# Performance work log

Hardware: AMD Instinct MI355X
Metric: run time of the kernel (lower is better)

Reference implementation:

```python
import jax, jax.numpy as jnp
import numpy as np

B, SEQ, S, DIM_IN, DIM_K, DIM_V = 4, 2048, 128, 512, 64, 64
L = SEQ + 2 * S
NEG = -1e30  # stand-in for log(0) in the tril mask (finite for stable vjp)


def _layernorm(x, g, b, eps=1e-5):
    m = jnp.mean(x, axis=-1, keepdims=True)
    v = jnp.var(x, axis=-1, keepdims=True)
    return (x - m) / jnp.sqrt(v + eps) * g + b


def setup_inputs() -> dict:
    key = jax.random.key(0)
    ks = jax.random.split(key, 18)
    w = lambda k, shape, s=0.02: (jax.random.normal(k, shape, jnp.float32) * s)
    inp = {
        "x": jax.random.normal(ks[0], (B, L, DIM_IN), jnp.float32),
        "Wq": w(ks[1], (DIM_IN, DIM_K)),
        "Wk": w(ks[2], (DIM_IN, DIM_K)),
        "Wv": w(ks[3], (DIM_IN, DIM_V)),
        "Wq_s": w(ks[4], (DIM_IN, DIM_K)),
        "Wk_s": w(ks[5], (DIM_IN, DIM_K)),
        "Wv_s": w(ks[6], (DIM_IN, DIM_V)),
        "Wq_e": w(ks[7], (DIM_IN, DIM_K)),
        "Wk_e": w(ks[8], (DIM_IN, DIM_K)),
        "Wv_e": w(ks[9], (DIM_IN, DIM_V)),
        "ln_g": jnp.ones((DIM_IN,), jnp.float32),
        "ln_b": jnp.zeros((DIM_IN,), jnp.float32),
        "ln_s_g": jnp.ones((DIM_IN,), jnp.float32),
        "ln_s_b": jnp.zeros((DIM_IN,), jnp.float32),
        "ln_e_g": jnp.ones((DIM_IN,), jnp.float32),
        "ln_e_b": jnp.zeros((DIM_IN,), jnp.float32),
        "cope_emb": jax.random.normal(ks[10], (DIM_K, S), jnp.float32),
        "offset": 0,
    }
    return inp


def reference(x, Wq, Wk, Wv, Wq_s, Wk_s, Wv_s, Wq_e, Wk_e, Wv_e,
              ln_g, ln_b, ln_s_g, ln_s_b, ln_e_g, ln_e_b, cope_emb, offset):
    # extract_state: first/last state_len tokens
    xs, xm, xe = x[:, :S], x[:, S:L - S], x[:, -S:]
    xm = _layernorm(xm, ln_g, ln_b)
    xs = _layernorm(xs, ln_s_g, ln_s_b)
    xe = _layernorm(xe, ln_e_g, ln_e_b)

    q, k, v = xm @ Wq, xm @ Wk, xm @ Wv          # (B, SEQ, dk/dv)
    q_s, k_s, v_s = xs @ Wq_s, xs @ Wk_s, xs @ Wv_s
    q_e, k_e, v_e = xe @ Wq_e, xe @ Wk_e, xe @ Wv_e

    # CoPE bias over the non-state block
    logits = jnp.einsum('bqd,bkd->bqk', q, k)    # (B, SEQ, SEQ)
    gates = jax.nn.sigmoid(logits)
    pos = jnp.flip(jnp.cumsum(jnp.flip(gates, -1), axis=-1), -1)
    pos = jnp.minimum(pos, jnp.float32(S - 1))
    pos_ceil = jnp.ceil(pos).astype(jnp.int32)
    pos_floor = jnp.floor(pos).astype(jnp.int32)
    logits_int = jnp.einsum('bqd,dk->bqk', q, cope_emb)  # (B, SEQ, S)
    logits_c = jnp.take_along_axis(logits_int, pos_ceil, axis=-1)
    logits_f = jnp.take_along_axis(logits_int, pos_floor, axis=-1)
    wfrac = pos - pos_floor.astype(pos.dtype)
    bias = logits_c * wfrac + logits_f * (1.0 - wfrac)   # (B, SEQ, SEQ)

    q_full = jnp.concatenate([q_s, q, q_e], axis=1)      # (B, L, dk)
    k_full = jnp.concatenate([k_s, k, k_e], axis=1)
    v_full = jnp.concatenate([v_s, v, v_e], axis=1)

    # explicit tril log-mask bias with CoPE injected in the middle block
    tri = jnp.tril(jnp.ones((L, L), dtype=bool))
    attn_bias = jnp.where(tri, 0.0, NEG).astype(jnp.float32)
    attn_bias = jnp.broadcast_to(attn_bias, (B, L, L))
    attn_bias = attn_bias.at[:, S:L - S, S:L - S].add(bias)

    scale = 1.0 / jnp.sqrt(jnp.float32(DIM_K))
    scores = jnp.einsum('bqd,bkd->bqk', q_full, k_full) * scale + attn_bias
    att = jax.nn.softmax(scores, axis=-1)
    return jnp.einsum('bqk,bkd->bqd', att, v_full)       # (B, L, dv)
```

## Files before the change

kernel.cpp:

```cpp
#include <hip/hip_runtime.h>
#include <math.h>

#define B_    4
#define SEQ_  2048
#define S_    128
#define L_    2304
#define DIN   512
#define DK    64
#define NEGINF (-1e30f)
#define SCALE 0.125f
#define NCOLS 2176
#define NMID  8192
#define NEDGE 1024
#define LE    2304
#define PROWS 4352

typedef _Float16 f16;
typedef __attribute__((ext_vector_type(8))) _Float16 half8;
typedef __attribute__((ext_vector_type(4))) float f32x4;

union U4 { uint4 u; f16 h[8]; };

__global__ __launch_bounds__(256) void k_ln(
    const float* __restrict__ x,
    const float* __restrict__ g0, const float* __restrict__ b0,
    const float* __restrict__ gs, const float* __restrict__ bs,
    const float* __restrict__ ge, const float* __restrict__ be,
    f16* __restrict__ xh, f16* __restrict__ xl)
{
    const int wave = threadIdx.x >> 6, lane = threadIdx.x & 63;
    const int row  = blockIdx.x * 4 + wave;
    const float4* xr = (const float4*)(x + (size_t)row * DIN);
    float4 v0 = xr[lane], v1 = xr[lane + 64];
    float s  = v0.x + v0.y + v0.z + v0.w + v1.x + v1.y + v1.z + v1.w;
    float s2 = v0.x*v0.x + v0.y*v0.y + v0.z*v0.z + v0.w*v0.w
             + v1.x*v1.x + v1.y*v1.y + v1.z*v1.z + v1.w*v1.w;
    #pragma unroll
    for (int m = 1; m < 64; m <<= 1) { s += __shfl_xor(s, m); s2 += __shfl_xor(s2, m); }
    float mean = s * (1.f / DIN);
    float var  = s2 * (1.f / DIN) - mean * mean;
    float rstd = rsqrtf(var + 1e-5f);

    const int r = row % L_;
    const float *gg, *bb;
    if (r < S_)            { gg = gs; bb = bs; }
    else if (r >= L_ - S_) { gg = ge; bb = be; }
    else                   { gg = g0; bb = b0; }
    float4 ga = ((const float4*)gg)[lane], gb = ((const float4*)gg)[lane + 64];
    float4 ba = ((const float4*)bb)[lane], bb4 = ((const float4*)bb)[lane + 64];

    float n0[4], n1[4];
    n0[0] = (v0.x - mean) * rstd * ga.x + ba.x;
    n0[1] = (v0.y - mean) * rstd * ga.y + ba.y;
    n0[2] = (v0.z - mean) * rstd * ga.z + ba.z;
    n0[3] = (v0.w - mean) * rstd * ga.w + ba.w;
    n1[0] = (v1.x - mean) * rstd * gb.x + bb4.x;
    n1[1] = (v1.y - mean) * rstd * gb.y + bb4.y;
    n1[2] = (v1.z - mean) * rstd * gb.z + bb4.z;
    n1[3] = (v1.w - mean) * rstd * gb.w + bb4.w;

    union { uint2 u; f16 h[4]; } h0, h1, l0, l1;
    #pragma unroll
    for (int i = 0; i < 4; ++i) {
        h0.h[i] = (f16)n0[i]; l0.h[i] = (f16)(n0[i] - (float)h0.h[i]);
        h1.h[i] = (f16)n1[i]; l1.h[i] = (f16)(n1[i] - (float)h1.h[i]);
    }
    f16* ph = xh + (size_t)row * DIN;
    f16* pl = xl + (size_t)row * DIN;
    *(uint2*)(ph + 4 * lane)       = h0.u;
    *(uint2*)(ph + 256 + 4 * lane) = h1.u;
    *(uint2*)(pl + 4 * lane)       = l0.u;
    *(uint2*)(pl + 256 + 4 * lane) = l1.u;
}

// ... 57 lines not shown
        __syncthreads();
        #pragma unroll
        for (int h = 0; h < 2; ++h) {
            half8 ah[2], al[2], bh[2], bl[2];
            #pragma unroll
            for (int rs = 0; rs < 2; ++rs) {
                const f16* base = As + (r0 + 16 * rs + cl) * 136 + h * 32 + quad * 8;
                ah[rs] = *(const half8*)(base);
                al[rs] = *(const half8*)(base + 64);
            }
            #pragma unroll
            for (int cs = 0; cs < 2; ++cs) {
                const f16* base = Bs + (c0 + 16 * cs + cl) * 136 + h * 32 + quad * 8;
                bh[cs] = *(const half8*)(base);
                bl[cs] = *(const half8*)(base + 64);
            }
            #pragma unroll
            for (int rs = 0; rs < 2; ++rs)
                #pragma unroll
                for (int cs = 0; cs < 2; ++cs) {
                    acc[rs][cs] = __builtin_amdgcn_mfma_f32_16x16x32_f16(ah[rs], bh[cs], acc[rs][cs], 0, 0, 0);
                    if (m < 2) {
                        acc[rs][cs] = __builtin_amdgcn_mfma_f32_16x16x32_f16(ah[rs], bl[cs], acc[rs][cs], 0, 0, 0);
                        acc[rs][cs] = __builtin_amdgcn_mfma_f32_16x16x32_f16(al[rs], bh[cs], acc[rs][cs], 0, 0, 0);
                    }
                }
        }
    }

    const int bI = row0 / L_;
    const int rb = row0 - bI * L_;
    f16* sp = (m == 0) ? qsp : ksp;
    #pragma unroll
    for (int rs = 0; rs < 2; ++rs)
        #pragma unroll
        for (int cs = 0; cs < 2; ++cs)
            #pragma unroll
            for (int r = 0; r < 4; ++r) {
                int lrow = r0 + 16 * rs + quad * 4 + r;
                int col  = c0 + 16 * cs + cl;
                float v  = acc[rs][cs][r];
                size_t grow = (size_t)(row0 + lrow);
                outf[grow * DK + col] = v;
                if (m < 2) {
                    f16 hv = (f16)v;
                    sp[grow * 128 + col]      = hv;
                    sp[grow * 128 + 64 + col] = (f16)(v - (float)hv);
                } else {
                    vhT[(size_t)(bI * 64 + col) * L_ + rb + lrow] = (f16)v;
                }
            }
}

__global__ __launch_bounds__(256) void k_dots(
    const f16* __restrict__ qsp, const f16* __restrict__ ksp,
    float* __restrict__ D)
{
    __shared__ f16 Qs[128 * 136];
    __shared__ f16 Ks[64 * 136];
    const int tid  = threadIdx.x;
    const int gr0  = blockIdx.x * 128;
    const int col0 = blockIdx.y * 64;
    const int b    = gr0 >> 11;
    const size_t qrow0 = (size_t)b * L_ + S_ + (gr0 & 2047);
    const size_t krow0 = (size_t)b * L_ + col0;

    #pragma unroll
    for (int i = 0; i < 8; ++i) {
        int g = tid + 256 * i;
        int r = g >> 4, c = g & 15;
        *(uint4*)(Qs + r * 136 + c * 8) = *(const uint4*)(qsp + (qrow0 + r) * 128 + c * 8);
    }
    #pragma unroll
    for (int i = 0; i < 4; ++i) {
        int g = tid + 256 * i;
        int r = g >> 4, c = g & 15;
        *(uint4*)(Ks + r * 136 + c * 8) = *(const uint4*)(ksp + (krow0 + r) * 128 + c * 8);
    }
    __syncthreads();

    const int w = tid >> 6, lane = tid & 63;
    const int cl = lane & 15, quad = lane >> 4;

    f32x4 acc[2][4];
    #pragma unroll
    for (int i = 0; i < 2; ++i)
        #pragma unroll
        for (int j = 0; j < 4; ++j) acc[i][j] = 0.f;

    #pragma unroll
    for (int h = 0; h < 2; ++h) {
        half8 ah[2], al[2], bh[4], bl[4];
        #pragma unroll
        for (int rs = 0; rs < 2; ++rs) {
            const f16* base = Qs + (32 * w + 16 * rs + cl) * 136 + h * 32 + quad * 8;
            ah[rs] = *(const half8*)(base);
            al[rs] = *(const half8*)(base + 64);
        }
        #pragma unroll
        for (int c = 0; c < 4; ++c) {
            const f16* base = Ks + (16 * c + cl) * 136 + h * 32 + quad * 8;
            bh[c] = *(const half8*)(base);
            bl[c] = *(const half8*)(base + 64);
        }
        #pragma unroll
        for (int rs = 0; rs < 2; ++rs)
            #pragma unroll
            for (int c = 0; c < 4; ++c) {
                acc[rs][c] = __builtin_amdgcn_mfma_f32_16x16x32_f16(ah[rs], bh[c], acc[rs][c], 0, 0, 0);
                acc[rs][c] = __builtin_amdgcn_mfma_f32_16x16x32_f16(ah[rs], bl[c], acc[rs][c], 0, 0, 0);
                acc[rs][c] = __builtin_amdgcn_mfma_f32_16x16x32_f16(al[rs], bh[c], acc[rs][c], 0, 0, 0);
            }
    }

    #pragma unroll
    for (int rs = 0; rs < 2; ++rs)
        #pragma unroll
        for (int c = 0; c < 4; ++c)
            #pragma unroll
            for (int r = 0; r < 4; ++r) {
                int mrow = gr0 + 32 * w + 16 * rs + quad * 4 + r;
                int n    = col0 + 16 * c + cl;
                D[(size_t)mrow * NCOLS + n] = acc[rs][c][r];
            }
}

__global__ __launch_bounds__(256) void k_scan(
    const float* __restrict__ qf, const float* __restrict__ cope,
    float* __restrict__ D)
{
    __shared__ float qv[DK];
    __shared__ float li[128];
    __shared__ float red[256];
    __shared__ float wtot[4];
    const int tid = threadIdx.x;
    const int gr  = blockIdx.x;
    const int b   = gr >> 11;
    const int q   = gr & 2047;
    const size_t grow = (size_t)b * L_ + S_ + q;

    if (tid < 16) ((float4*)qv)[tid] = ((const float4*)qf)[grow * 16 + tid];
    __syncthreads();
    if (tid < 128) {
        float a = 0.f;
        #pragma unroll
        for (int d = 0; d < DK; ++d) a += qv[d] * cope[d * S_ + tid];
        li[tid] = a;
    }

    const float* Dr = D + (size_t)gr * NCOLS;
    const int j0 = tid * 8;
    float dot[8], gte[8];
    *(float4*)&dot[0] = *(const float4*)(Dr + 128 + j0);
    *(float4*)&dot[4] = *(const float4*)(Dr + 128 + j0 + 4);
    float sv = (tid < 128) ? Dr[tid] * SCALE : NEGINF;

    float csum = 0.f;
    #pragma unroll
    for (int jj = 0; jj < 8; ++jj) {
        gte[jj] = 1.f / (1.f + __expf(-dot[jj]));
        csum += gte[jj];
    }
    const int lane = tid & 63, wid = tid >> 6;
    float inc = csum;
    #pragma unroll
    for (int off = 1; off < 64; off <<= 1) {
        float u = __shfl_down(inc, off, 64);
        if (lane + off < 64) inc += u;
    }
    if (lane == 0) wtot[wid] = inc;
    __syncthreads();
    float wsuf = 0.f;
    #pragma unroll
    for (int w = 0; w < 4; ++w) if (w > wid) wsuf += wtot[w];
    float run = inc - csum + wsuf;

    float p8[8];
    #pragma unroll
    for (int jj = 7; jj >= 0; --jj) {
        run += gte[jj];
        float pos = fminf(run, (float)(S_ - 1));
        float pfl = floorf(pos);
        int ic  = (int)ceilf(pos);
        int ifl = (int)pfl;
        float w = pos - pfl;
        float bias = li[ic] * w + li[ifl] * (1.f - w);
        p8[jj] = (j0 + jj <= q) ? dot[jj] * SCALE + bias : NEGINF;
    }

    float mx = sv;
    #pragma unroll
    for (int jj = 0; jj < 8; ++jj) mx = fmaxf(mx, p8[jj]);
    red[tid] = mx;
    __syncthreads();
    for (int off = 128; off > 0; off >>= 1) {
        if (tid < off) red[tid] = fmaxf(red[tid], red[tid + off]);
        __syncthreads();
    }
    mx = red[0];
    __syncthreads();

    float lsum = 0.f;
    float e8[8];
    #pragma unroll
    for (int jj = 0; jj < 8; ++jj) {
        e8[jj] = __expf(p8[jj] - mx);
        lsum += e8[jj];
    }
    float es = 0.f;
    if (tid < 128) { es = __expf(sv - mx); lsum += es; }
    red[tid] = lsum;
    __syncthreads();
    for (int off = 128; off > 0; off >>= 1) {
        if (tid < off) red[tid] += red[tid + off];
        __syncthreads();
    }
    float inv = 1.f / red[0];

    f16* pb = (f16*)D + (size_t)gr * PROWS;
    const int qlim = (q & ~63) + 64;
    if (j0 < qlim) {
        U4 o;
        #pragma unroll
        for (int jj = 0; jj < 8; ++jj) o.h[jj] = (f16)(e8[jj] * inv);
        *(uint4*)(pb + 128 + j0) = o.u;
    }
    if (tid < 128) pb[tid] = (f16)(es * inv);
}

__global__ __launch_bounds__(256) void k_pv(
    const f16* __restrict__ Pb, const f16* __restrict__ vhT,
    float* __restrict__ Opart)
{
    __shared__ f16 Ps[64 * 72];
    __shared__ f16 Vt[64 * 72];
    const int tid = threadIdx.x;
    const int gr0 = blockIdx.x * 64;
    const int ks  = blockIdx.y;
    const int b   = gr0 >> 11, q0 = gr0 & 2047;
    const int cmax  = (191 + q0) >> 6;
    const int c_beg = ks * 9;
    int c_end = c_beg + 9;
    if (c_end > 34) c_end = 34;
    if (c_end > cmax + 1) c_end = cmax + 1;

    const int w = tid >> 6, lane = tid & 63;
    const int cl = lane & 15, quad = lane >> 4;
    f32x4 acc[4];
    #pragma unroll
    for (int c = 0; c < 4; ++c) acc[c] = 0.f;

    for (int ch = c_beg; ch < c_end; ++ch) {
        __syncthreads();
        #pragma unroll
        for (int i = 0; i < 2; ++i) {
            int g = tid + 256 * i;
            int r = g >> 3, c = g & 7;
            *(uint4*)(Ps + r * 72 + c * 8) =
                *(const uint4*)(Pb + (size_t)(gr0 + r) * PROWS + ch * 64 + c * 8);
            *(uint4*)(Vt + r * 72 + c * 8) =
                *(const uint4*)(vhT + (size_t)(b * 64 + r) * L_ + ch * 64 + c * 8);
        }
        __syncthreads();
        #pragma unroll
        for (int h = 0; h < 2; ++h) {
            half8 a = *(const half8*)(Ps + (16 * w + cl) * 72 + h * 32 + quad * 8);
            #pragma unroll
            for (int c = 0; c < 4; ++c) {
                half8 bv = *(const half8*)(Vt + (16 * c + cl) * 72 + h * 32 + quad * 8);
                acc[c] = __builtin_amdgcn_mfma_f32_16x16x32_f16(a, bv, acc[c], 0, 0, 0);
            }
        }
    }
    #pragma unroll
    for (int c = 0; c < 4; ++c)
        #pragma unroll
        for (int r = 0; r < 4; ++r) {
            int mrow = gr0 + 16 * w + quad * 4 + r;
            int n    = 16 * c + cl;
            Opart[((size_t)ks * NMID + mrow) * DK + n] = acc[c][r];
        }
}

__global__ __launch_bounds__(256) void k_merge(
    const float* __restrict__ Opart, float* __restrict__ out)
{
    const int e  = blockIdx.x * 256 + threadIdx.x;
    const int gr = e >> 6, c = e & 63;
    const int b  = gr >> 11, q = gr & 2047;
    const int NP = NMID * DK;
    float s = Opart[e] + Opart[e + NP] + Opart[e + 2 * NP] + Opart[e + 3 * NP];
    out[((size_t)b * L_ + S_ + q) * DK + c] = s;
}

__global__ __launch_bounds__(256) void k_dots_edge(
    const float* __restrict__ qf, const float* __restrict__ kf,
    float* __restrict__ De)
{
    const int bx   = blockIdx.x;
    const int b    = bx >> 1;
    const int half = bx & 1;
    const int col0 = blockIdx.y * 128;
    if (half == 0 && col0 > 127) return;

    __shared__ float Qs[128 * 68];
    __shared__ float Kt[64 * 136];
    const int tid = threadIdx.x;
    const int er0 = bx * 128;
    const size_t qrow0 = (size_t)b * L_ + (half ? 2176 : 0);
    const size_t krow0 = (size_t)b * L_ + col0;

    #pragma unroll
    for (int i = 0; i < 8; ++i) {
        int g = tid + 256 * i;
        int r = g >> 4, f = g & 15;
        *(float4*)(Qs + r * 68 + f * 4) = ((const float4*)qf)[(qrow0 + r) * 16 + f];
    }
    #pragma unroll
    for (int i = 0; i < 8; ++i) {
        int g = tid + 256 * i;
        int j = g >> 4, f = g & 15;
        float4 kv = ((const float4*)kf)[(krow0 + j) * 16 + f];
        Kt[(f * 4 + 0) * 136 + j] = kv.x;
        Kt[(f * 4 + 1) * 136 + j] = kv.y;
        Kt[(f * 4 + 2) * 136 + j] = kv.z;
        Kt[(f * 4 + 3) * 136 + j] = kv.w;
    }
    __syncthreads();

    const int c8 = tid & 15, r8 = tid >> 4;
    float acc[8][8] = {};
    for (int d0 = 0; d0 < 64; d0 += 4) {
        float4 a[8];
        #pragma unroll
        for (int i = 0; i < 8; ++i)
            a[i] = *(const float4*)(Qs + (r8 * 8 + i) * 68 + d0);
        #pragma unroll
        for (int dd = 0; dd < 4; ++dd) {
            float4 k0 = *(const float4*)(Kt + (d0 + dd) * 136 + c8 * 8);
            float4 k1 = *(const float4*)(Kt + (d0 + dd) * 136 + c8 * 8 + 4);
            #pragma unroll
            for (int i = 0; i < 8; ++i) {
                float av = (dd == 0) ? a[i].x : (dd == 1) ? a[i].y : (dd == 2) ? a[i].z : a[i].w;
                acc[i][0] += av * k0.x; acc[i][1] += av * k0.y;
                acc[i][2] += av * k0.z; acc[i][3] += av * k0.w;
                acc[i][4] += av * k1.x; acc[i][5] += av * k1.y;
                acc[i][6] += av * k1.z; acc[i][7] += av * k1.w;
            }
        }
    }
    #pragma unroll
    for (int i = 0; i < 8; ++i) {
        size_t o = (size_t)(er0 + r8 * 8 + i) * LE + col0 + c8 * 8;
        *(float4*)(De + o)     = make_float4(acc[i][0], acc[i][1], acc[i][2], acc[i][3]);
        *(float4*)(De + o + 4) = make_float4(acc[i][4], acc[i][5], acc[i][6], acc[i][7]);
    }
}

__global__ __launch_bounds__(256) void k_soft_edge(float* __restrict__ De)
{
    __shared__ float red[256];
    const int tid = threadIdx.x;
    const int er  = blockIdx.x;
    const int r   = er & 255;
    const int Q   = (r < 128) ? r : (2048 + r);
    const size_t rowoff = (size_t)er * LE;

    float v[9];
    #pragma unroll
    for (int i = 0; i < 9; ++i) {
        int j = tid + 256 * i;
        float d = De[rowoff + j];
        v[i] = (j <= Q) ? d * SCALE : NEGINF;
    }
    float mx = v[0];
    #pragma unroll
    for (int i = 1; i < 9; ++i) mx = fmaxf(mx, v[i]);
    red[tid] = mx;
    __syncthreads();
    for (int off = 128; off > 0; off >>= 1) {
        if (tid < off) red[tid] = fmaxf(red[tid], red[tid + off]);
        __syncthreads();
    }
    mx = red[0];
    __syncthreads();

    float lsum = 0.f;
    #pragma unroll
    for (int i = 0; i < 9; ++i) {
        v[i] = __expf(v[i] - mx);
        lsum += v[i];
    }
    red[tid] = lsum;
    __syncthreads();
    for (int off = 128; off > 0; off >>= 1) {
        if (tid < off) red[tid] += red[tid + off];
        __syncthreads();
    }
    float inv = 1.f / red[0];
    #pragma unroll
    for (int i = 0; i < 9; ++i)
        De[rowoff + tid + 256 * i] = v[i] * inv;
}

__global__ __launch_bounds__(256) void k_pv_edge(
    const float* __restrict__ De, const float* __restrict__ vf,
    float* __restrict__ Oe)
{
    __shared__ float Ps[32 * 68];
    __shared__ float Vs[64 * 68];
    const int tid = threadIdx.x;
    const int er0 = blockIdx.x * 32;
    const int ks  = blockIdx.y;
    const int b   = er0 >> 8, r0 = er0 & 255;
    const int Qmax = (r0 < 128) ? (r0 + 31) : (2048 + r0 + 31);
    const int cmax = Qmax >> 6;
    const int c_beg = ks * 9;
    int c_end = c_beg + 9;
    if (c_end > 36) c_end = 36;
    if (c_end > cmax + 1) c_end = cmax + 1;

    const int c4 = tid & 15, rg = tid >> 4;
    float acc[2][4] = {};

    for (int ch = c_beg; ch < c_end; ++ch) {
        __syncthreads();
        #pragma unroll
        for (int i = 0; i < 2; ++i) {
            int g = tid + 256 * i;
            int r = g >> 4, f = g & 15;
            *(float4*)(Ps + r * 68 + f * 4) =
                *(const float4*)(De + (size_t)(er0 + r) * LE + ch * 64 + f * 4);
        }
        #pragma unroll
        for (int i = 0; i < 4; ++i) {
            int g = tid + 256 * i;
            int j = g >> 4, f = g & 15;
            *(float4*)(Vs + j * 68 + f * 4) =
                *(const float4*)(vf + (size_t)(b * L_ + ch * 64 + j) * DK + f * 4);
        }
        __syncthreads();
        #pragma unroll 4
        for (int j = 0; j < 64; ++j) {
            float4 vv = *(const float4*)(Vs + j * 68 + c4 * 4);
            float p0 = Ps[(rg * 2 + 0) * 68 + j];
            float p1 = Ps[(rg * 2 + 1) * 68 + j];
            acc[0][0] += p0 * vv.x; acc[0][1] += p0 * vv.y;
            acc[0][2] += p0 * vv.z; acc[0][3] += p0 * vv.w;
            acc[1][0] += p1 * vv.x; acc[1][1] += p1 * vv.y;
            acc[1][2] += p1 * vv.z; acc[1][3] += p1 * vv.w;
        }
    }
    #pragma unroll
    for (int i = 0; i < 2; ++i)
        *(float4*)(Oe + ((size_t)ks * NEDGE + er0 + rg * 2 + i) * DK + c4 * 4) =
            make_float4(acc[i][0], acc[i][1], acc[i][2], acc[i][3]);
}

__global__ __launch_bounds__(256) void k_merge_edge(
    const float* __restrict__ Oe, float* __restrict__ out)
{
    const int e  = blockIdx.x * 256 + threadIdx.x;
    const int er = e >> 6, c = e & 63;
    const int b  = er >> 8, r = er & 255;
    const int gQ = (r < 128) ? r : (2048 + r);
    const int NP = NEDGE * DK;
    float s = Oe[e] + Oe[e + NP] + Oe[e + 2 * NP] + Oe[e + 3 * NP];
    out[((size_t)b * L_ + gQ) * DK + c] = s;
}

extern "C" void kernel_launch(void* const* d_in, const int* in_sizes, int n_in,
                              void* d_out, int out_size, void* d_ws, size_t ws_size,
                              hipStream_t stream)
{
    const float* x    = (const float*)d_in[0];
    const float* Wq   = (const float*)d_in[1];
    const float* Wk   = (const float*)d_in[2];
    const float* Wv   = (const float*)d_in[3];
    const float* Wqs  = (const float*)d_in[4];
    const float* Wks  = (const float*)d_in[5];
    const float* Wvs  = (const float*)d_in[6];
    const float* Wqe  = (const float*)d_in[7];
    const float* Wke  = (const float*)d_in[8];
    const float* Wve  = (const float*)d_in[9];
    const float* g0   = (const float*)d_in[10];
    const float* b0   = (const float*)d_in[11];
    const float* gs   = (const float*)d_in[12];
    const float* bs   = (const float*)d_in[13];
    const float* ge   = (const float*)d_in[14];
    const float* be   = (const float*)d_in[15];
    const float* cope = (const float*)d_in[16];

    const size_t NR = (size_t)B_ * L_;
    float* ws = (float*)d_ws;
    float* qf    = ws;
    float* kf    = qf + NR * DK;
    float* vf    = kf + NR * DK;
    float* Opart = vf + NR * DK;
    f16*   qsp   = (f16*)(Opart + (size_t)4 * NMID * DK);
    f16*   ksp   = qsp + NR * 128;
    f16*   vhT   = ksp + NR * 128;
    float* D     = (float*)(vhT + NR * DK);
    f16*   xh    = (f16*)D;
    f16*   xl    = xh + NR * DIN;
    float* De    = D;
    float* Oe    = Opart;
    float* out   = (float*)d_out;

    k_ln  <<<L_ * B_ / 4, 256, 0, stream>>>(x, g0, b0, gs, bs, ge, be, xh, xl);
    k_proj<<<dim3(144, 3), 256, 0, stream>>>(xh, xl, Wq, Wk, Wv, Wqs, Wks, Wvs,
                                             Wqe, Wke, Wve, qf, kf, vf,
                                             qsp, ksp, vhT);
    k_dots<<<dim3(NMID / 128, NCOLS / 64), 256, 0, stream>>>(qsp, ksp, D);
    k_scan<<<NMID, 256, 0, stream>>>(qf, cope, D);
    k_pv  <<<dim3(NMID / 64, 4), 256, 0, stream>>>((const f16*)D, vhT, Opart);
    k_merge<<<NMID * DK / 256, 256, 0, stream>>>(Opart, out);
    k_dots_edge<<<dim3(8, 18), 256, 0, stream>>>(qf, kf, De);
    k_soft_edge<<<NEDGE, 256, 0, stream>>>(De);
    k_pv_edge<<<dim3(NEDGE / 32, 4), 256, 0, stream>>>(De, vf, Oe);
    k_merge_edge<<<NEDGE * DK / 256, 256, 0, stream>>>(Oe, out);
}
```

Measured before the change: 230.6 us.

## Replace materialized score matrix with flash-style fused attention and chunked gate suffix sums

Measured after the change: 258.7 us. +12.2%, slower.

```diff
diff --git a/kernel.cpp b/kernel.cpp
--- a/kernel.cpp
+++ b/kernel.cpp
@@ -13,13 +13,10 @@
 #define NMID  8192
 #define NEDGE 1024
 #define LE    2304
-#define PROWS 4352
 
 typedef _Float16 f16;
 typedef __attribute__((ext_vector_type(8))) _Float16 half8;
 typedef __attribute__((ext_vector_type(4))) float f32x4;
-
-union U4 { uint4 u; f16 h[8]; };
 
 __global__ __launch_bounds__(256) void k_ln(
     const float* __restrict__ x,
@@ -183,18 +180,51 @@
             }
 }
 
-__global__ __launch_bounds__(256) void k_dots(
+__global__ __launch_bounds__(256) void k_cope(
+    const float* __restrict__ qf, const float* __restrict__ cope,
+    float* __restrict__ Li)
+{
+    __shared__ float qs[32 * 68];
+    const int tid = threadIdx.x;
+    const int gr0 = blockIdx.x * 32;
+    const int b   = gr0 >> 11;
+    const size_t qrow0 = (size_t)b * L_ + S_ + (gr0 & 2047);
+    #pragma unroll
+    for (int i = 0; i < 2; ++i) {
+        int g = tid + 256 * i;
+        int r = g >> 4, f = g & 15;
+        *(float4*)(qs + r * 68 + f * 4) = ((const float4*)qf)[(qrow0 + r) * 16 + f];
+    }
+    __syncthreads();
+    const int c4 = tid & 31, r4 = tid >> 5;
+    float acc[4][4] = {};
+    for (int d = 0; d < DK; ++d) {
+        float4 cv = ((const float4*)cope)[d * 32 + c4];
+        #pragma unroll
+        for (int i = 0; i < 4; ++i) {
+            float a = qs[(r4 * 4 + i) * 68 + d];
+            acc[i][0] += a * cv.x; acc[i][1] += a * cv.y;
+            acc[i][2] += a * cv.z; acc[i][3] += a * cv.w;
+        }
+    }
+    #pragma unroll
+    for (int i = 0; i < 4; ++i)
+        *(float4*)(Li + (size_t)(gr0 + r4 * 4 + i) * 128 + c4 * 4) =
+            make_float4(acc[i][0], acc[i][1], acc[i][2], acc[i][3]);
+}
+
+__global__ __launch_bounds__(256) void k_gates(
     const f16* __restrict__ qsp, const f16* __restrict__ ksp,
-    float* __restrict__ D)
+    float* __restrict__ G)
 {
     __shared__ f16 Qs[128 * 136];
     __shared__ f16 Ks[64 * 136];
-    const int tid  = threadIdx.x;
-    const int gr0  = blockIdx.x * 128;
-    const int col0 = blockIdx.y * 64;
-    const int b    = gr0 >> 11;
+    const int tid = threadIdx.x;
+    const int gr0 = blockIdx.x * 128;
+    const int chm = blockIdx.y;
+    const int b   = gr0 >> 11;
     const size_t qrow0 = (size_t)b * L_ + S_ + (gr0 & 2047);
-    const size_t krow0 = (size_t)b * L_ + col0;
+    const size_t krow0 = (size_t)b * L_ + S_ + chm * 64;
 
     #pragma unroll
     for (int i = 0; i < 8; ++i) {
@@ -247,181 +277,248 @@
     #pragma unroll
     for (int rs = 0; rs < 2; ++rs)
         #pragma unroll
-        for (int c = 0; c < 4; ++c)
-            #pragma unroll
-            for (int r = 0; r < 4; ++r) {
-                int mrow = gr0 + 32 * w + 16 * rs + quad * 4 + r;
-                int n    = col0 + 16 * c + cl;
-                D[(size_t)mrow * NCOLS + n] = acc[rs][c][r];
-            }
-}
-
-__global__ __launch_bounds__(256) void k_scan(
-    const float* __restrict__ qf, const float* __restrict__ cope,
-    float* __restrict__ D)
-{
-    __shared__ float qv[DK];
-    __shared__ float li[128];
-    __shared__ float red[256];
-    __shared__ float wtot[4];
-    const int tid = threadIdx.x;
-    const int gr  = blockIdx.x;
-    const int b   = gr >> 11;
-    const int q   = gr & 2047;
-    const size_t grow = (size_t)b * L_ + S_ + q;
-
-    if (tid < 16) ((float4*)qv)[tid] = ((const float4*)qf)[grow * 16 + tid];
-    __syncthreads();
-    if (tid < 128) {
-        float a = 0.f;
-        #pragma unroll
-        for (int d = 0; d < DK; ++d) a += qv[d] * cope[d * S_ + tid];
-        li[tid] = a;
-    }
-
-    const float* Dr = D + (size_t)gr * NCOLS;
-    const int j0 = tid * 8;
-    float dot[8], gte[8];
-    *(float4*)&dot[0] = *(const float4*)(Dr + 128 + j0);
-    *(float4*)&dot[4] = *(const float4*)(Dr + 128 + j0 + 4);
-    float sv = (tid < 128) ? Dr[tid] * SCALE : NEGINF;
-
-    float csum = 0.f;
-    #pragma unroll
-    for (int jj = 0; jj < 8; ++jj) {
-        gte[jj] = 1.f / (1.f + __expf(-dot[jj]));
-        csum += gte[jj];
-    }
-    const int lane = tid & 63, wid = tid >> 6;
-    float inc = csum;
-    #pragma unroll
-    for (int off = 1; off < 64; off <<= 1) {
-        float u = __shfl_down(inc, off, 64);
-        if (lane + off < 64) inc += u;
-    }
-    if (lane == 0) wtot[wid] = inc;
-    __syncthreads();
-    float wsuf = 0.f;
-    #pragma unroll
-    for (int w = 0; w < 4; ++w) if (w > wid) wsuf += wtot[w];
-    float run = inc - csum + wsuf;
-
-    float p8[8];
-    #pragma unroll
-    for (int jj = 7; jj >= 0; --jj) {
-        run += gte[jj];
-        float pos = fminf(run, (float)(S_ - 1));
-        float pfl = floorf(pos);
-        int ic  = (int)ceilf(pos);
-        int ifl = (int)pfl;
-        float w = pos - pfl;
-        float bias = li[ic] * w + li[ifl] * (1.f - w);
-        p8[jj] = (j0 + jj <= q) ? dot[jj] * SCALE + bias : NEGINF;
-    }
-
-    float mx = sv;
-    #pragma unroll
-    for (int jj = 0; jj < 8; ++jj) mx = fmaxf(mx, p8[jj]);
-    red[tid] = mx;
-    __syncthreads();
-    for (int off = 128; off > 0; off >>= 1) {
-        if (tid < off) red[tid] = fmaxf(red[tid], red[tid + off]);
-        __syncthreads();
-    }
-    mx = red[0];
-    __syncthreads();
-
-    float lsum = 0.f;
-    float e8[8];
-    #pragma unroll
-    for (int jj = 0; jj < 8; ++jj) {
-        e8[jj] = __expf(p8[jj] - mx);
-        lsum += e8[jj];
-    }
-    float es = 0.f;
-    if (tid < 128) { es = __expf(sv - mx); lsum += es; }
-    red[tid] = lsum;
-    __syncthreads();
-    for (int off = 128; off > 0; off >>= 1) {
-        if (tid < off) red[tid] += red[tid + off];
-        __syncthreads();
-    }
-    float inv = 1.f / red[0];
-
-    f16* pb = (f16*)D + (size_t)gr * PROWS;
-    const int qlim = (q & ~63) + 64;
-    if (j0 < qlim) {
-        U4 o;
-        #pragma unroll
-        for (int jj = 0; jj < 8; ++jj) o.h[jj] = (f16)(e8[jj] * inv);
-        *(uint4*)(pb + 128 + j0) = o.u;
-    }
-    if (tid < 128) pb[tid] = (f16)(es * inv);
-}
-
-__global__ __launch_bounds__(256) void k_pv(
-    const f16* __restrict__ Pb, const f16* __restrict__ vhT,
-    float* __restrict__ Opart)
-{
-    __shared__ f16 Ps[64 * 72];
-    __shared__ f16 Vt[64 * 72];
+        for (int r = 0; r < 4; ++r) {
+            float s = 0.f;
+            #pragma unroll
+            for (int c = 0; c < 4; ++c)
+                s += 1.f / (1.f + __expf(-acc[rs][c][r]));
+            #pragma unroll
+            for (int off = 1; off < 16; off <<= 1) s += __shfl_xor(s, off);
+            if (cl == 0)
+                G[(size_t)(gr0 + 32 * w + 16 * rs + quad * 4 + r) * 32 + chm] = s;
+        }
+}
+
+__global__ __launch_bounds__(256) void k_suffix(
+    const float* __restrict__ G, float* __restrict__ R)
+{
+    const int row = blockIdx.x * 256 + threadIdx.x;
+    float v[32];
+    #pragma unroll
+    for (int i = 0; i < 8; ++i)
+        *(float4*)&v[i * 4] = ((const float4*)G)[(size_t)row * 8 + i];
+    float run = 0.f;
+    #pragma unroll
+    for (int ch = 31; ch >= 0; --ch) { float t = v[ch]; v[ch] = run; run += t; }
+    #pragma unroll
+    for (int i = 0; i < 8; ++i)
+        ((float4*)R)[(size_t)row * 8 + i] = *(const float4*)&v[i * 4];
+}
+
+__global__ __launch_bounds__(256) void k_flash(
+    const f16* __restrict__ qsp, const f16* __restrict__ ksp,
+    const f16* __restrict__ vhT, const float* __restrict__ Li,
+    const float* __restrict__ R,
+    float* __restrict__ Opart, float2* __restrict__ Ml)
+{
+    __shared__ f16  Qs[64 * 136];
+    __shared__ f16  Ks[64 * 136];
+    __shared__ f16  Ps[64 * 72];
+    __shared__ f16  Vt[64 * 72];
+    __shared__ f16  LiS[64 * 128];
+    __shared__ float Rs[64 * 32];
+
     const int tid = threadIdx.x;
     const int gr0 = blockIdx.x * 64;
     const int ks  = blockIdx.y;
     const int b   = gr0 >> 11, q0 = gr0 & 2047;
-    const int cmax  = (191 + q0) >> 6;
+    const size_t qrow0 = (size_t)b * L_ + S_ + q0;
+
+    const int cmax = (191 + q0) >> 6;
     const int c_beg = ks * 9;
     int c_end = c_beg + 9;
     if (c_end > 34) c_end = 34;
     if (c_end > cmax + 1) c_end = cmax + 1;
 
+    #pragma unroll
+    for (int i = 0; i < 4; ++i) {
+        int g = tid + 256 * i;
+        int r = g >> 4, c = g & 15;
+        *(uint4*)(Qs + r * 136 + c * 8) = *(const uint4*)(qsp + (qrow0 + r) * 128 + c * 8);
+    }
+    #pragma unroll
+    for (int i = 0; i < 8; ++i) {
+        int g = tid + 256 * i;
+        int r = g >> 5, c4 = g & 31;
+        float4 lv = ((const float4*)Li)[(size_t)(gr0 + r) * 32 + c4];
+        LiS[r * 128 + c4 * 4 + 0] = (f16)lv.x;
+        LiS[r * 128 + c4 * 4 + 1] = (f16)lv.y;
+        LiS[r * 128 + c4 * 4 + 2] = (f16)lv.z;
+        LiS[r * 128 + c4 * 4 + 3] = (f16)lv.w;
+    }
+    #pragma unroll
+    for (int i = 0; i < 2; ++i) {
+        int g = tid + 256 * i;
+        int r = g >> 3, c4 = g & 7;
+        ((float4*)Rs)[r * 8 + c4] = ((const float4*)R)[(size_t)(gr0 + r) * 8 + c4];
+    }
+
     const int w = tid >> 6, lane = tid & 63;
     const int cl = lane & 15, quad = lane >> 4;
-    f32x4 acc[4];
-    #pragma unroll
-    for (int c = 0; c < 4; ++c) acc[c] = 0.f;
+
+    float m4[4], l4[4];
+    f32x4 oacc[4];
+    #pragma unroll
+    for (int r = 0; r < 4; ++r) { m4[r] = NEGINF; l4[r] = 0.f; }
+    #pragma unroll
+    for (int cd = 0; cd < 4; ++cd) oacc[cd] = 0.f;
 
     for (int ch = c_beg; ch < c_end; ++ch) {
         __syncthreads();
+        #pragma unroll
+        for (int i = 0; i < 4; ++i) {
+            int g = tid + 256 * i;
+            int r = g >> 4, c = g & 15;
+            *(uint4*)(Ks + r * 136 + c * 8) =
+                *(const uint4*)(ksp + (size_t)(b * L_ + 64 * ch + r) * 128 + c * 8);
+        }
         #pragma unroll
         for (int i = 0; i < 2; ++i) {
             int g = tid + 256 * i;
             int r = g >> 3, c = g & 7;
-            *(uint4*)(Ps + r * 72 + c * 8) =
-                *(const uint4*)(Pb + (size_t)(gr0 + r) * PROWS + ch * 64 + c * 8);
             *(uint4*)(Vt + r * 72 + c * 8) =
-                *(const uint4*)(vhT + (size_t)(b * 64 + r) * L_ + ch * 64 + c * 8);
-        }
-        __syncthreads();
+                *(const uint4*)(vhT + (size_t)(b * 64 + r) * L_ + 64 * ch + c * 8);
+        }
+        __syncthreads();
+
+        f32x4 d[4];
+        #pragma unroll
+        for (int c = 0; c < 4; ++c) d[c] = 0.f;
+        #pragma unroll
+        for (int h = 0; h < 2; ++h) {
+            const f16* abase = Qs + (16 * w + cl) * 136 + h * 32 + quad * 8;
+            half8 ah = *(const half8*)(abase);
+            half8 al = *(const half8*)(abase + 64);
+            #pragma unroll
+            for (int c = 0; c < 4; ++c) {
+                const f16* bbase = Ks + (16 * c + cl) * 136 + h * 32 + quad * 8;
+                half8 bh = *(const half8*)(bbase);
+                half8 bl = *(const half8*)(bbase + 64);
+                d[c] = __builtin_amdgcn_mfma_f32_16x16x32_f16(ah, bh, d[c], 0, 0, 0);
+                d[c] = __builtin_amdgcn_mfma_f32_16x16x32_f16(ah, bl, d[c], 0, 0, 0);
+                d[c] = __builtin_amdgcn_mfma_f32_16x16x32_f16(al, bh, d[c], 0, 0, 0);
+            }
+        }
+
+        if (ch >= 2) {
+            const int chm = ch - 2;
+            float ts[4][4], incl[4][4];
+            #pragma unroll
+            for (int c = 0; c < 4; ++c)
+                #pragma unroll
+                for (int r = 0; r < 4; ++r) {
+                    float gg = 1.f / (1.f + __expf(-d[c][r]));
+                    float inc = gg;
+                    #pragma unroll
+                    for (int off = 1; off < 16; off <<= 1) {
+                        float u = __shfl_down(inc, off);
+                        if (cl + off < 16) inc += u;
+                    }
+                    incl[c][r] = inc;
+                    ts[c][r]   = __shfl(inc, quad << 4);
+                }
+            #pragma unroll
+            for (int r = 0; r < 4; ++r) {
+                const int lr = 16 * w + quad * 4 + r;
+                float T[4];
+                T[3] = 0.f;
+                T[2] = ts[3][r];
+                T[1] = T[2] + ts[2][r];
+                T[0] = T[1] + ts[1][r];
+                float rsuf = Rs[lr * 32 + chm];
+                #pragma unroll
+                for (int c = 0; c < 4; ++c) {
+                    float suf = incl[c][r] + T[c] + rsuf;
+                    float pos = fminf(suf, (float)(S_ - 1));
+                    int   ifl = (int)pos;
+                    int   ic  = (int)ceilf(pos);
+                    float wfr = pos - (float)ifl;
+                    float bias = (float)LiS[lr * 128 + ic] * wfr
+                               + (float)LiS[lr * 128 + ifl] * (1.f - wfr);
+                    int jmid = 64 * ch + 16 * c + cl - 128;
+                    d[c][r] = (jmid <= q0 + lr) ? d[c][r] * SCALE + bias : NEGINF;
+                }
+            }
+        } else {
+            #pragma unroll
+            for (int c = 0; c < 4; ++c)
+                #pragma unroll
+                for (int r = 0; r < 4; ++r) d[c][r] *= SCALE;
+        }
+
+        #pragma unroll
+        for (int r = 0; r < 4; ++r) {
+            float mx = d[0][r];
+            #pragma unroll
+            for (int c = 1; c < 4; ++c) mx = fmaxf(mx, d[c][r]);
+            #pragma unroll
+            for (int off = 1; off < 16; off <<= 1) mx = fmaxf(mx, __shfl_xor(mx, off));
+            float mnew  = fmaxf(m4[r], mx);
+            float alpha = __expf(m4[r] - mnew);
+            m4[r] = mnew;
+            float es = 0.f;
+            #pragma unroll
+            for (int c = 0; c < 4; ++c) {
+                float e = (d[c][r] <= -1e29f) ? 0.f : __expf(d[c][r] - mnew);
+                Ps[(16 * w + quad * 4 + r) * 72 + 16 * c + cl] = (f16)e;
+                es += e;
+            }
+            #pragma unroll
+            for (int off = 1; off < 16; off <<= 1) es += __shfl_xor(es, off);
+            l4[r] = l4[r] * alpha + es;
+            #pragma unroll
+            for (int cd = 0; cd < 4; ++cd) oacc[cd][r] *= alpha;
+        }
+        __syncthreads();
+
         #pragma unroll
         for (int h = 0; h < 2; ++h) {
             half8 a = *(const half8*)(Ps + (16 * w + cl) * 72 + h * 32 + quad * 8);
             #pragma unroll
-            for (int c = 0; c < 4; ++c) {
-                half8 bv = *(const half8*)(Vt + (16 * c + cl) * 72 + h * 32 + quad * 8);
-                acc[c] = __builtin_amdgcn_mfma_f32_16x16x32_f16(a, bv, acc[c], 0, 0, 0);
-            }
-        }
-    }
-    #pragma unroll
-    for (int c = 0; c < 4; ++c)
+            for (int cd = 0; cd < 4; ++cd) {
+                half8 bv = *(const half8*)(Vt + (16 * cd + cl) * 72 + h * 32 + quad * 8);
+                oacc[cd] = __builtin_amdgcn_mfma_f32_16x16x32_f16(a, bv, oacc[cd], 0, 0, 0);
+            }
+        }
+    }
+
+    #pragma unroll
+    for (int cd = 0; cd < 4; ++cd)
         #pragma unroll
         for (int r = 0; r < 4; ++r) {
             int mrow = gr0 + 16 * w + quad * 4 + r;
-            int n    = 16 * c + cl;
-            Opart[((size_t)ks * NMID + mrow) * DK + n] = acc[c][r];
-        }
+            Opart[((size_t)ks * NMID + mrow) * DK + 16 * cd + cl] = oacc[cd][r];
+        }
+    if (cl == 0) {
+        #pragma unroll
+        for (int r = 0; r < 4; ++r) {
+            int mrow = gr0 + 16 * w + quad * 4 + r;
+            Ml[(size_t)ks * NMID + mrow] = make_float2(m4[r], l4[r]);
+        }
+    }
 }
 
 __global__ __launch_bounds__(256) void k_merge(
-    const float* __restrict__ Opart, float* __restrict__ out)
+    const float* __restrict__ Opart, const float2* __restrict__ Ml,
+    float* __restrict__ out)
 {
     const int e  = blockIdx.x * 256 + threadIdx.x;
     const int gr = e >> 6, c = e & 63;
     const int b  = gr >> 11, q = gr & 2047;
-    const int NP = NMID * DK;
-    float s = Opart[e] + Opart[e + NP] + Opart[e + 2 * NP] + Opart[e + 3 * NP];
-    out[((size_t)b * L_ + S_ + q) * DK + c] = s;
+    float2 ml[4];
+    #pragma unroll
+    for (int i = 0; i < 4; ++i) ml[i] = Ml[(size_t)i * NMID + gr];
+    float M = ml[0].x;
+    #pragma unroll
+    for (int i = 1; i < 4; ++i) M = fmaxf(M, ml[i].x);
+    float num = 0.f, den = 0.f;
+    #pragma unroll
+    for (int i = 0; i < 4; ++i) {
+        float sc = __expf(ml[i].x - M);
+        den += sc * ml[i].y;
+        num += sc * Opart[((size_t)i * NMID + gr) * DK + c];
+    }
+    out[((size_t)b * L_ + S_ + q) * DK + c] = num / den;
 }
 
 __global__ __launch_bounds__(256) void k_dots_edge(
@@ -628,13 +725,16 @@
     float* kf    = qf + NR * DK;
     float* vf    = kf + NR * DK;
     float* Opart = vf + NR * DK;
-    f16*   qsp   = (f16*)(Opart + (size_t)4 * NMID * DK);
+    float2* Ml   = (float2*)(Opart + (size_t)4 * NMID * DK);
+    float* Li    = (float*)(Ml + (size_t)4 * NMID);
+    float* G     = Li + (size_t)NMID * 128;
+    float* R     = G + (size_t)NMID * 32;
+    f16*   qsp   = (f16*)(R + (size_t)NMID * 32);
     f16*   ksp   = qsp + NR * 128;
     f16*   vhT   = ksp + NR * 128;
-    float* D     = (float*)(vhT + NR * DK);
-    f16*   xh    = (f16*)D;
+    float* De    = (float*)(vhT + NR * DK);
+    f16*   xh    = (f16*)De;
     f16*   xl    = xh + NR * DIN;
-    float* De    = D;
     float* Oe    = Opart;
     float* out   = (float*)d_out;
 
@@ -642,10 +742,11 @@
     k_proj<<<dim3(144, 3), 256, 0, stream>>>(xh, xl, Wq, Wk, Wv, Wqs, Wks, Wvs,
                                              Wqe, Wke, Wve, qf, kf, vf,
                                              qsp, ksp, vhT);
-    k_dots<<<dim3(NMID / 128, NCOLS / 64), 256, 0, stream>>>(qsp, ksp, D);
-    k_scan<<<NMID, 256, 0, stream>>>(qf, cope, D);
-    k_pv  <<<dim3(NMID / 64, 4), 256, 0, stream>>>((const f16*)D, vhT, Opart);
-    k_merge<<<NMID * DK / 256, 256, 0, stream>>>(Opart, out);
+    k_cope<<<NMID / 32, 256, 0, stream>>>(qf, cope, Li);
+    k_gates<<<dim3(NMID / 128, 32), 256, 0, stream>>>(qsp, ksp, G);
+    k_suffix<<<NMID / 256, 256, 0, stream>>>(G, R);
+    k_flash<<<dim3(NMID / 64, 4), 256, 0, stream>>>(qsp, ksp, vhT, Li, R, Opart, Ml);
+    k_merge<<<NMID * DK / 256, 256, 0, stream>>>(Opart, Ml, out);
     k_dots_edge<<<dim3(8, 18), 256, 0, stream>>>(qf, kf, De);
     k_soft_edge<<<NEDGE, 256, 0, stream>>>(De);
     k_pv_edge<<<dim3(NEDGE / 32, 4), 256, 0, stream>>>(De, vf, Oe);
```

## Precompute per-chunk gate sums in dots kernel; skip masked writes; MFMA edge path

Applied to the files above, without the earlier changes.

Result: faster. 223.2 us (-3.2%).

```diff
diff --git a/kernel.cpp b/kernel.cpp
--- a/kernel.cpp
+++ b/kernel.cpp
@@ -14,6 +14,7 @@
 #define NEDGE 1024
 #define LE    2304
 #define PROWS 4352
+#define PEPITCH 4608
 
 typedef _Float16 f16;
 typedef __attribute__((ext_vector_type(8))) _Float16 half8;
@@ -185,15 +186,17 @@
 
 __global__ __launch_bounds__(256) void k_dots(
     const f16* __restrict__ qsp, const f16* __restrict__ ksp,
-    float* __restrict__ D)
+    float* __restrict__ D, float* __restrict__ G)
 {
     __shared__ f16 Qs[128 * 136];
     __shared__ f16 Ks[64 * 136];
     const int tid  = threadIdx.x;
     const int gr0  = blockIdx.x * 128;
-    const int col0 = blockIdx.y * 64;
+    const int by   = blockIdx.y;
+    const int col0 = by * 64;
     const int b    = gr0 >> 11;
-    const size_t qrow0 = (size_t)b * L_ + S_ + (gr0 & 2047);
+    const int q0   = gr0 & 2047;
+    const size_t qrow0 = (size_t)b * L_ + S_ + q0;
     const size_t krow0 = (size_t)b * L_ + col0;
 
     #pragma unroll
@@ -244,33 +247,55 @@
             }
     }
 
-    #pragma unroll
-    for (int rs = 0; rs < 2; ++rs)
-        #pragma unroll
-        for (int c = 0; c < 4; ++c)
+    const bool writeD = (by < 2) || ((by - 2) <= (q0 >> 6) + 1);
+    if (writeD) {
+        #pragma unroll
+        for (int rs = 0; rs < 2; ++rs)
+            #pragma unroll
+            for (int c = 0; c < 4; ++c)
+                #pragma unroll
+                for (int r = 0; r < 4; ++r) {
+                    int mrow = gr0 + 32 * w + 16 * rs + quad * 4 + r;
+                    int n    = col0 + 16 * c + cl;
+                    D[(size_t)mrow * NCOLS + n] = acc[rs][c][r];
+                }
+    }
+    if (by >= 2) {
+        const int chm = by - 2;
+        #pragma unroll
+        for (int rs = 0; rs < 2; ++rs)
             #pragma unroll
             for (int r = 0; r < 4; ++r) {
-                int mrow = gr0 + 32 * w + 16 * rs + quad * 4 + r;
-                int n    = col0 + 16 * c + cl;
-                D[(size_t)mrow * NCOLS + n] = acc[rs][c][r];
-            }
+                float s = 0.f;
+                #pragma unroll
+                for (int c = 0; c < 4; ++c)
+                    s += 1.f / (1.f + __expf(-acc[rs][c][r]));
+                #pragma unroll
+                for (int off = 1; off < 16; off <<= 1) s += __shfl_xor(s, off);
+                if (cl == 0)
+                    G[(size_t)(gr0 + 32 * w + 16 * rs + quad * 4 + r) * 32 + chm] = s;
+            }
+    }
 }
 
 __global__ __launch_bounds__(256) void k_scan(
     const float* __restrict__ qf, const float* __restrict__ cope,
-    float* __restrict__ D)
+    const float* __restrict__ G, float* __restrict__ D)
 {
     __shared__ float qv[DK];
     __shared__ float li[128];
     __shared__ float red[256];
     __shared__ float wtot[4];
+    __shared__ float Gs[32];
     const int tid = threadIdx.x;
     const int gr  = blockIdx.x;
     const int b   = gr >> 11;
     const int q   = gr & 2047;
     const size_t grow = (size_t)b * L_ + S_ + q;
+    const int qlim = (q & ~63) + 64;
 
     if (tid < 16) ((float4*)qv)[tid] = ((const float4*)qf)[grow * 16 + tid];
+    if (tid >= 16 && tid < 24) ((float4*)Gs)[tid - 16] = ((const float4*)G)[(size_t)gr * 8 + tid - 16];
     __syncthreads();
     if (tid < 128) {
         float a = 0.f;
@@ -282,16 +307,21 @@
     const float* Dr = D + (size_t)gr * NCOLS;
     const int j0 = tid * 8;
     float dot[8], gte[8];
-    *(float4*)&dot[0] = *(const float4*)(Dr + 128 + j0);
-    *(float4*)&dot[4] = *(const float4*)(Dr + 128 + j0 + 4);
+    float csum = 0.f;
+    if (j0 < qlim) {
+        *(float4*)&dot[0] = *(const float4*)(Dr + 128 + j0);
+        *(float4*)&dot[4] = *(const float4*)(Dr + 128 + j0 + 4);
+        #pragma unroll
+        for (int jj = 0; jj < 8; ++jj) {
+            gte[jj] = 1.f / (1.f + __expf(-dot[jj]));
+            csum += gte[jj];
+        }
+    } else {
+        #pragma unroll
+        for (int jj = 0; jj < 8; ++jj) { dot[jj] = 0.f; gte[jj] = 0.f; }
+    }
     float sv = (tid < 128) ? Dr[tid] * SCALE : NEGINF;
 
-    float csum = 0.f;
-    #pragma unroll
-    for (int jj = 0; jj < 8; ++jj) {
-        gte[jj] = 1.f / (1.f + __expf(-dot[jj]));
-        csum += gte[jj];
-    }
     const int lane = tid & 63, wid = tid >> 6;
     float inc = csum;
     #pragma unroll
@@ -304,7 +334,9 @@
     float wsuf = 0.f;
     #pragma unroll
     for (int w = 0; w < 4; ++w) if (w > wid) wsuf += wtot[w];
-    float run = inc - csum + wsuf;
+    float tail = 0.f;
+    for (int c = (q >> 6) + 1; c < 32; ++c) tail += Gs[c];
+    float run = inc - csum + wsuf + tail;
 
     float p8[8];
     #pragma unroll
@@ -349,7 +381,6 @@
     float inv = 1.f / red[0];
 
     f16* pb = (f16*)D + (size_t)gr * PROWS;
-    const int qlim = (q & ~63) + 64;
     if (j0 < qlim) {
         U4 o;
         #pragma unroll
@@ -425,67 +456,80 @@
 }
 
 __global__ __launch_bounds__(256) void k_dots_edge(
-    const float* __restrict__ qf, const float* __restrict__ kf,
+    const f16* __restrict__ qsp, const f16* __restrict__ ksp,
     float* __restrict__ De)
 {
     const int bx   = blockIdx.x;
     const int b    = bx >> 1;
     const int half = bx & 1;
-    const int col0 = blockIdx.y * 128;
-    if (half == 0 && col0 > 127) return;
-
-    __shared__ float Qs[128 * 68];
-    __shared__ float Kt[64 * 136];
+    const int by   = blockIdx.y;
+    if (half == 0 && by > 1) return;
+
+    __shared__ f16 Qs[128 * 136];
+    __shared__ f16 Ks[64 * 136];
     const int tid = threadIdx.x;
     const int er0 = bx * 128;
     const size_t qrow0 = (size_t)b * L_ + (half ? 2176 : 0);
-    const size_t krow0 = (size_t)b * L_ + col0;
+    const size_t krow0 = (size_t)b * L_ + by * 64;
 
     #pragma unroll
     for (int i = 0; i < 8; ++i) {
         int g = tid + 256 * i;
-        int r = g >> 4, f = g & 15;
-        *(float4*)(Qs + r * 68 + f * 4) = ((const float4*)qf)[(qrow0 + r) * 16 + f];
-    }
-    #pragma unroll
-    for (int i = 0; i < 8; ++i) {
+        int r = g >> 4, c = g & 15;
+        *(uint4*)(Qs + r * 136 + c * 8) = *(const uint4*)(qsp + (qrow0 + r) * 128 + c * 8);
+    }
+    #pragma unroll
+    for (int i = 0; i < 4; ++i) {
         int g = tid + 256 * i;
-        int j = g >> 4, f = g & 15;
-        float4 kv = ((const float4*)kf)[(krow0 + j) * 16 + f];
-        Kt[(f * 4 + 0) * 136 + j] = kv.x;
-        Kt[(f * 4 + 1) * 136 + j] = kv.y;
-        Kt[(f * 4 + 2) * 136 + j] = kv.z;
-        Kt[(f * 4 + 3) * 136 + j] = kv.w;
-    }
-    __syncthreads();
-
-    const int c8 = tid & 15, r8 = tid >> 4;
-    float acc[8][8] = {};
-    for (int d0 = 0; d0 < 64; d0 += 4) {
-        float4 a[8];
-        #pragma unroll
-        for (int i = 0; i < 8; ++i)
-            a[i] = *(const float4*)(Qs + (r8 * 8 + i) * 68 + d0);
-        #pragma unroll
-        for (int dd = 0; dd < 4; ++dd) {
-            float4 k0 = *(const float4*)(Kt + (d0 + dd) * 136 + c8 * 8);
-            float4 k1 = *(const float4*)(Kt + (d0 + dd) * 136 + c8 * 8 + 4);
-            #pragma unroll
-            for (int i = 0; i < 8; ++i) {
-                float av = (dd == 0) ? a[i].x : (dd == 1) ? a[i].y : (dd == 2) ? a[i].z : a[i].w;
-                acc[i][0] += av * k0.x; acc[i][1] += av * k0.y;
-                acc[i][2] += av * k0.z; acc[i][3] += av * k0.w;
-                acc[i][4] += av * k1.x; acc[i][5] += av * k1.y;
-                acc[i][6] += av * k1.z; acc[i][7] += av * k1.w;
-            }
-        }
-    }
-    #pragma unroll
-    for (int i = 0; i < 8; ++i) {
-        size_t o = (size_t)(er0 + r8 * 8 + i) * LE + col0 + c8 * 8;
-        *(float4*)(De + o)     = make_float4(acc[i][0], acc[i][1], acc[i][2], acc[i][3]);
-        *(float4*)(De + o + 4) = make_float4(acc[i][4], acc[i][5], acc[i][6], acc[i][7]);
-    }
+        int r = g >> 4, c = g & 15;
+        *(uint4*)(Ks + r * 136 + c * 8) = *(const uint4*)(ksp + (krow0 + r) * 128 + c * 8);
+    }
+    __syncthreads();
+
+    const int w = tid >> 6, lane = tid & 63;
+    const int cl = lane & 15, quad = lane >> 4;
+
+    f32x4 acc[2][4];
+    #pragma unroll
+    for (int i = 0; i < 2; ++i)
+        #pragma unroll
+        for (int j = 0; j < 4; ++j) acc[i][j] = 0.f;
+
+    #pragma unroll
+    for (int h = 0; h < 2; ++h) {
+        half8 ah[2], al[2], bh[4], bl[4];
+        #pragma unroll
+        for (int rs = 0; rs < 2; ++rs) {
+            const f16* base = Qs + (32 * w + 16 * rs + cl) * 136 + h * 32 + quad * 8;
+            ah[rs] = *(const half8*)(base);
+            al[rs] = *(const half8*)(base + 64);
+        }
+        #pragma unroll
+        for (int c = 0; c < 4; ++c) {
+            const f16* base = Ks + (16 * c + cl) * 136 + h * 32 + quad * 8;
+            bh[c] = *(const half8*)(base);
+            bl[c] = *(const half8*)(base + 64);
+        }
+        #pragma unroll
+        for (int rs = 0; rs < 2; ++rs)
+            #pragma unroll
+            for (int c = 0; c < 4; ++c) {
+                acc[rs][c] = __builtin_amdgcn_mfma_f32_16x16x32_f16(ah[rs], bh[c], acc[rs][c], 0, 0, 0);
+                acc[rs][c] = __builtin_amdgcn_mfma_f32_16x16x32_f16(ah[rs], bl[c], acc[rs][c], 0, 0, 0);
+                acc[rs][c] = __builtin_amdgcn_mfma_f32_16x16x32_f16(al[rs], bh[c], acc[rs][c], 0, 0, 0);
+            }
+    }
+
+    #pragma unroll
+    for (int rs = 0; rs < 2; ++rs)
+        #pragma unroll
+        for (int c = 0; c < 4; ++c)
+            #pragma unroll
+            for (int r = 0; r < 4; ++r) {
+                int erow = er0 + 32 * w + 16 * rs + quad * 4 + r;
+                int n    = by * 64 + 16 * c + cl;
+                De[(size_t)erow * LE + n] = acc[rs][c][r];
+            }
 }
 
 __global__ __launch_bounds__(256) void k_soft_edge(float* __restrict__ De)
@@ -529,63 +573,65 @@
         __syncthreads();
     }
     float inv = 1.f / red[0];
+    f16* pe = (f16*)De + (size_t)er * PEPITCH;
     #pragma unroll
     for (int i = 0; i < 9; ++i)
-        De[rowoff + tid + 256 * i] = v[i] * inv;
+        pe[tid + 256 * i] = (f16)(v[i] * inv);
 }
 
 __global__ __launch_bounds__(256) void k_pv_edge(
-    const float* __restrict__ De, const float* __restrict__ vf,
+    const f16* __restrict__ Pe, const f16* __restrict__ vhT,
     float* __restrict__ Oe)
 {
-    __shared__ float Ps[32 * 68];
-    __shared__ float Vs[64 * 68];
+    __shared__ f16 Ps[64 * 72];
+    __shared__ f16 Vt[64 * 72];
     const int tid = threadIdx.x;
-    const int er0 = blockIdx.x * 32;
+    const int er0 = blockIdx.x * 64;
     const int ks  = blockIdx.y;
     const int b   = er0 >> 8, r0 = er0 & 255;
-    const int Qmax = (r0 < 128) ? (r0 + 31) : (2048 + r0 + 31);
+    const int Qmax = (r0 < 128) ? (r0 + 63) : (2048 + r0 + 63);
     const int cmax = Qmax >> 6;
-    const int c_beg = ks * 9;
-    int c_end = c_beg + 9;
+    const int c_beg = ks * 5;
+    int c_end = c_beg + 5;
     if (c_end > 36) c_end = 36;
     if (c_end > cmax + 1) c_end = cmax + 1;
 
-    const int c4 = tid & 15, rg = tid >> 4;
-    float acc[2][4] = {};
+    const int w = tid >> 6, lane = tid & 63;
+    const int cl = lane & 15, quad = lane >> 4;
+    f32x4 acc[4];
+    #pragma unroll
+    for (int c = 0; c < 4; ++c) acc[c] = 0.f;
 
     for (int ch = c_beg; ch < c_end; ++ch) {
         __syncthreads();
         #pragma unroll
         for (int i = 0; i < 2; ++i) {
             int g = tid + 256 * i;
-            int r = g >> 4, f = g & 15;
-            *(float4*)(Ps + r * 68 + f * 4) =
-                *(const float4*)(De + (size_t)(er0 + r) * LE + ch * 64 + f * 4);
-        }
-        #pragma unroll
-        for (int i = 0; i < 4; ++i) {
-            int g = tid + 256 * i;
-            int j = g >> 4, f = g & 15;
-            *(float4*)(Vs + j * 68 + f * 4) =
-                *(const float4*)(vf + (size_t)(b * L_ + ch * 64 + j) * DK + f * 4);
-        }
-        __syncthreads();
-        #pragma unroll 4
-        for (int j = 0; j < 64; ++j) {
-            float4 vv = *(const float4*)(Vs + j * 68 + c4 * 4);
-            float p0 = Ps[(rg * 2 + 0) * 68 + j];
-            float p1 = Ps[(rg * 2 + 1) * 68 + j];
-            acc[0][0] += p0 * vv.x; acc[0][1] += p0 * vv.y;
-            acc[0][2] += p0 * vv.z; acc[0][3] += p0 * vv.w;
-            acc[1][0] += p1 * vv.x; acc[1][1] += p1 * vv.y;
-            acc[1][2] += p1 * vv.z; acc[1][3] += p1 * vv.w;
-        }
-    }
-    #pragma unroll
-    for (int i = 0; i < 2; ++i)
-        *(float4*)(Oe + ((size_t)ks * NEDGE + er0 + rg * 2 + i) * DK + c4 * 4) =
-            make_float4(acc[i][0], acc[i][1], acc[i][2], acc[i][3]);
+            int r = g >> 3, c = g & 7;
+            *(uint4*)(Ps + r * 72 + c * 8) =
+                *(const uint4*)(Pe + (size_t)(er0 + r) * PEPITCH + ch * 64 + c * 8);
+            *(uint4*)(Vt + r * 72 + c * 8) =
+                *(const uint4*)(vhT + (size_t)(b * 64 + r) * L_ + ch * 64 + c * 8);
+        }
+        __syncthreads();
+        #pragma unroll
+        for (int h = 0; h < 2; ++h) {
+            half8 a = *(const half8*)(Ps + (16 * w + cl) * 72 + h * 32 + quad * 8);
+            #pragma unroll
+            for (int c = 0; c < 4; ++c) {
+                half8 bv = *(const half8*)(Vt + (16 * c + cl) * 72 + h * 32 + quad * 8);
+                acc[c] = __builtin_amdgcn_mfma_f32_16x16x32_f16(a, bv, acc[c], 0, 0, 0);
+            }
+        }
+    }
+    #pragma unroll
+    for (int c = 0; c < 4; ++c)
+        #pragma unroll
+        for (int r = 0; r < 4; ++r) {
+            int erow = er0 + 16 * w + quad * 4 + r;
+            int n    = 16 * c + cl;
+            Oe[((size_t)ks * NEDGE + erow) * DK + n] = acc[c][r];
+        }
 }
 
 __global__ __launch_bounds__(256) void k_merge_edge(
@@ -596,7 +642,9 @@
     const int b  = er >> 8, r = er & 255;
     const int gQ = (r < 128) ? r : (2048 + r);
     const int NP = NEDGE * DK;
-    float s = Oe[e] + Oe[e + NP] + Oe[e + 2 * NP] + Oe[e + 3 * NP];
+    float s = 0.f;
+    #pragma unroll
+    for (int i = 0; i < 8; ++i) s += Oe[e + i * NP];
     out[((size_t)b * L_ + gQ) * DK + c] = s;
 }
 
@@ -628,7 +676,8 @@
     float* kf    = qf + NR * DK;
     float* vf    = kf + NR * DK;
     float* Opart = vf + NR * DK;
-    f16*   qsp   = (f16*)(Opart + (size_t)4 * NMID * DK);
+    float* G     = Opart + (size_t)4 * NMID * DK;
+    f16*   qsp   = (f16*)(G + (size_t)NMID * 32);
     f16*   ksp   = qsp + NR * 128;
     f16*   vhT   = ksp + NR * 128;
     float* D     = (float*)(vhT + NR * DK);
@@ -642,12 +691,12 @@
     k_proj<<<dim3(144, 3), 256, 0, stream>>>(xh, xl, Wq, Wk, Wv, Wqs, Wks, Wvs,
                                              Wqe, Wke, Wve, qf, kf, vf,
                                              qsp, ksp, vhT);
-    k_dots<<<dim3(NMID / 128, NCOLS / 64), 256, 0, stream>>>(qsp, ksp, D);
-    k_scan<<<NMID, 256, 0, stream>>>(qf, cope, D);
+    k_dots<<<dim3(NMID / 128, 34), 256, 0, stream>>>(qsp, ksp, D, G);
+    k_scan<<<NMID, 256, 0, stream>>>(qf, cope, G, D);
     k_pv  <<<dim3(NMID / 64, 4), 256, 0, stream>>>((const f16*)D, vhT, Opart);
     k_merge<<<NMID * DK / 256, 256, 0, stream>>>(Opart, out);
-    k_dots_edge<<<dim3(8, 18), 256, 0, stream>>>(qf, kf, De);
+    k_dots_edge<<<dim3(8, 36), 256, 0, stream>>>(qsp, ksp, De);
     k_soft_edge<<<NEDGE, 256, 0, stream>>>(De);
-    k_pv_edge<<<dim3(NEDGE / 32, 4), 256, 0, stream>>>(De, vf, Oe);
+    k_pv_edge<<<dim3(NEDGE / 64, 8), 256, 0, stream>>>((const f16*)De, vhT, Oe);
     k_merge_edge<<<NEDGE * DK / 256, 256, 0, stream>>>(Oe, out);
 }
```
